# Performance work log

Hardware: AMD Instinct MI355X
Metric: run time of the kernel (lower is better)

## Reference

```python
import jax, jax.numpy as jnp
import numpy as np

NA, NH, E, EL, D = 100000, 20000, 1000000, 200000, 128


def _sage(x_src, x_dst, src, dst, W_l, b_l, W_r, num_dst):
    # PyG SAGEConv: out = lin_l(mean_j x_src[j]) + lin_r(x_dst); lin_l has bias, lin_r does not.
    msg = x_src[src]                                   # [E, D] gather
    agg = jax.ops.segment_sum(msg, dst, num_segments=num_dst)   # [num_dst, D]
    deg = jax.ops.segment_sum(jnp.ones((src.shape[0],), x_src.dtype), dst, num_segments=num_dst)
    agg = agg / jnp.maximum(deg, 1.0)[:, None]         # mean aggregation; isolated nodes -> 0
    return agg @ W_l + b_l + x_dst @ W_r


def setup_inputs() -> dict:
    key = jax.random.key(0)
    ks = jax.random.split(key, 24)
    s = 1.0 / np.sqrt(D)
    inp = {
        "x_author": jax.random.normal(ks[0], (NA, D), jnp.float32),
        "x_hotel": jax.random.normal(ks[1], (NH, D), jnp.float32),
        "ei_ah_src": jax.random.randint(ks[2], (E,), 0, NA, jnp.int32),
        "ei_ah_dst": jax.random.randint(ks[3], (E,), 0, NH, jnp.int32),
        "ei_ha_src": jax.random.randint(ks[4], (E,), 0, NH, jnp.int32),
        "ei_ha_dst": jax.random.randint(ks[5], (E,), 0, NA, jnp.int32),
        "eli_row": jax.random.randint(ks[6], (EL,), 0, NA, jnp.int32),
        "eli_col": jax.random.randint(ks[7], (EL,), 0, NH, jnp.int32),
    }
    # per-layer, per-edge-type SAGE weights
    names = ["W1_ah_l", "W1_ah_r", "W1_ha_l", "W1_ha_r", "W2_ah_l", "W2_ah_r", "W2_ha_l", "W2_ha_r"]
    for i, n in enumerate(names):
        inp[n] = jax.random.normal(ks[8 + i], (D, D), jnp.float32) * s
    inp["b1_ah_l"] = jnp.zeros((D,), jnp.float32)
    inp["b1_ha_l"] = jnp.zeros((D,), jnp.float32)
    inp["b2_ah_l"] = jnp.zeros((D,), jnp.float32)
    inp["b2_ha_l"] = jnp.zeros((D,), jnp.float32)
    # decoder MLP
    inp["W_lin1"] = jax.random.normal(ks[16], (2 * D, D), jnp.float32) * (1.0 / np.sqrt(2 * D))
    inp["b_lin1"] = jnp.zeros((D,), jnp.float32)
    inp["W_lin2"] = jax.random.normal(ks[17], (D, 1), jnp.float32) * s
    inp["b_lin2"] = jnp.zeros((1,), jnp.float32)
    return inp


def reference(x_author, x_hotel, ei_ah_src, ei_ah_dst, ei_ha_src, ei_ha_dst,
              eli_row, eli_col,
              W1_ah_l, b1_ah_l, W1_ah_r, W1_ha_l, b1_ha_l, W1_ha_r,
              W2_ah_l, b2_ah_l, W2_ah_r, W2_ha_l, b2_ha_l, W2_ha_r,
              W_lin1, b_lin1, W_lin2, b_lin2):
    # layer 1 (HeteroConv: each node type receives from exactly one edge type) + relu
    h_hotel = jax.nn.relu(_sage(x_author, x_hotel, ei_ah_src, ei_ah_dst, W1_ah_l, b1_ah_l, W1_ah_r, NH))
    h_author = jax.nn.relu(_sage(x_hotel, x_author, ei_ha_src, ei_ha_dst, W1_ha_l, b1_ha_l, W1_ha_r, NA))
    # layer 2 (no relu on last layer)
    z_hotel = _sage(h_author, h_hotel, ei_ah_src, ei_ah_dst, W2_ah_l, b2_ah_l, W2_ah_r, NH)
    z_author = _sage(h_hotel, h_author, ei_ha_src, ei_ha_dst, W2_ha_l, b2_ha_l, W2_ha_r, NA)
    # edge decoder: gather-concat -> 2-layer MLP
    z1 = jnp.concatenate([z_author[eli_row], z_hotel[eli_col]], axis=-1)  # [EL, 2D]
    z2 = jax.nn.relu(z1 @ W_lin1 + b_lin1)                                # [EL, D]
    pred = (z2 @ W_lin2 + b_lin2).reshape(-1)                             # [EL]
    return (pred, z1, z2)
```

## Files before the change

### kernel.cpp

```cpp
#include <hip/hip_runtime.h>

#define NA_ 100000
#define NH_ 20000
#define E_  1000000
#define EL_ 200000
#define D_  128

#define NBH_ 20
#define NBA_ 98
#define NBT_ 118

#define FBH_ 313
#define FBA_ 1563

typedef __attribute__((ext_vector_type(8))) short short8;
typedef __attribute__((ext_vector_type(4))) float f32x4;

__device__ __forceinline__ ushort f2bf(float f) {
  union { float f; uint u; } v; v.f = f;
  uint u = v.u;
  return (ushort)((u + 0x7FFFu + ((u >> 16) & 1u)) >> 16);
}
__device__ __forceinline__ uint pack2bf(float a, float b) {
  return (uint)f2bf(a) | ((uint)f2bf(b) << 16);
}


__global__ __launch_bounds__(256) void cvt_count_k(const float* __restrict__ xa, ushort* __restrict__ da,
                                                   const float* __restrict__ xh, ushort* __restrict__ dh,
                                                   const int* __restrict__ d1, int* __restrict__ c1,
                                                   const int* __restrict__ d2, int* __restrict__ c2) {
  int i = blockIdx.x * 256 + threadIdx.x;
  if (i < E_) atomicAdd(&c1[d1[i]], 1);
  else if (i < 2 * E_) atomicAdd(&c2[d2[i - E_]], 1);
  const int na4 = NA_ * 32;
  if (i < na4) {
    float4 v = *(const float4*)(xa + (size_t)i * 4);
    ((uint2*)da)[i] = make_uint2(pack2bf(v.x, v.y), pack2bf(v.z, v.w));
  } else {
    int k = i - na4;
    if (k < NH_ * 32) {
      float4 v = *(const float4*)(xh + (size_t)k * 4);
      ((uint2*)dh)[k] = make_uint2(pack2bf(v.x, v.y), pack2bf(v.z, v.w));
    }
  }
}


__global__ __launch_bounds__(256) void csr_partial_k(const int* __restrict__ cnt_h,
                                                     const int* __restrict__ cnt_a,
                                                     int* __restrict__ partials) {
  int b = blockIdx.x;
  bool isH = b < NBH_;
  const int* c = isH ? cnt_h : cnt_a;
  int n = isH ? NH_ : NA_;
  int chunk = isH ? b : b - NBH_;
  int t = threadIdx.x;
  int i0 = chunk * 1024 + t * 4;
  int s = 0;
  if (i0 + 3 < n) {
    int4 v = *(const int4*)(c + i0);
    s = v.x + v.y + v.z + v.w;
  } else {
    for (int k = 0; k < 4; k++) if (i0 + k < n) s += c[i0 + k];
  }
#pragma unroll
  for (int d = 1; d < 64; d <<= 1) s += __shfl_xor(s, d);
  __shared__ int ws[4];
  int lane = t & 63, wv = t >> 6;
  if (lane == 0) ws[wv] = s;
  __syncthreads();
  if (t == 0) partials[b] = ws[0] + ws[1] + ws[2] + ws[3];
}

__global__ __launch_bounds__(128) void csr_scanp_k(int* __restrict__ partials,
                                                   int* __restrict__ off_h,
                                                   int* __restrict__ off_a) {
  __shared__ int s[128];
  int t = threadIdx.x;
  int orig = (t < NBT_) ? partials[t] : 0;
  int seg = (t < NBH_) ? 0 : 1;
  s[t] = orig;
  __syncthreads();
  for (int d = 1; d < 128; d <<= 1) {
    int v = 0;
    if (t >= d) {
      int o = t - d;
      if (((o < NBH_) ? 0 : 1) == seg) v = s[o];
    }
    __syncthreads();
    s[t] += v;
    __syncthreads();
  }
  if (t < NBT_) partials[t] = s[t] - orig;
  if (t == 0) { off_h[NH_] = E_; off_a[NA_] = E_; }
}

__global__ __launch_bounds__(256) void csr_scatter_k(int* __restrict__ cnt_h, int* __restrict__ off_h,
                                                     int* __restrict__ cnt_a, int* __restrict__ off_a,
                                                     const int* __restrict__ partials) {
  int b = blockIdx.x;
  bool isH = b < NBH_;
  int* c = isH ? cnt_h : cnt_a;
  int* off = isH ? off_h : off_a;
  int n = isH ? NH_ : NA_;
  int chunk = isH ? b : b - NBH_;
  int t = threadIdx.x, lane = t & 63, wv = t >> 6;
  int base = partials[b];
  int i0 = chunk * 1024 + t * 4;
  int v0 = 0, v1 = 0, v2 = 0, v3 = 0;
  if (i0 + 3 < n) {
    int4 v = *(const int4*)(c + i0);
    v0 = v.x; v1 = v.y; v2 = v.z; v3 = v.w;
  } else {
    if (i0 < n) v0 = c[i0];
    if (i0 + 1 < n) v1 = c[i0 + 1];
    if (i0 + 2 < n) v2 = c[i0 + 2];
    if (i0 + 3 < n) v3 = c[i0 + 3];
  }
  int tsum = v0 + v1 + v2 + v3;
  int x = tsum;
#pragma unroll
  for (int d = 1; d < 64; d <<= 1) { int y = __shfl_up(x, d); if (lane >= d) x += y; }
  __shared__ int ws[4], wb[4];
  if (lane == 63) ws[wv] = x;
  __syncthreads();
  if (t == 0) { int r = 0; for (int i = 0; i < 4; i++) { wb[i] = r; r += ws[i]; } }
  __syncthreads();
  int run = base + wb[wv] + (x - tsum);
  int o0 = run, o1 = o0 + v0, o2 = o1 + v1, o3 = o2 + v2;
  if (i0 + 3 < n) {
    *(int4*)(off + i0) = make_int4(o0, o1, o2, o3);
    *(int4*)(c + i0) = make_int4(o0, o1, o2, o3);
  } else {
    if (i0 < n) { off[i0] = o0; c[i0] = o0; }
    if (i0 + 1 < n) { off[i0 + 1] = o1; c[i0 + 1] = o1; }
    if (i0 + 2 < n) { off[i0 + 2] = o2; c[i0 + 2] = o2; }
    if (i0 + 3 < n) { off[i0 + 3] = o3; c[i0 + 3] = o3; }
  }
}

__global__ void fill_edges_k(const int* __restrict__ s1, const int* __restrict__ d1,
                             int* __restrict__ cur1, int* __restrict__ out1,
                             const int* __restrict__ s2, const int* __restrict__ d2,
                             int* __restrict__ cur2, int* __restrict__ out2) {
  int i = blockIdx.x * 256 + threadIdx.x;
  if (i < E_) {
    int p = atomicAdd(&cur1[d1[i]], 1);
    out1[p] = s1[i];
  } else if (i < 2 * E_) {
    int ii = i - E_;
    int p = atomicAdd(&cur2[d2[ii]], 1);
    out2[p] = s2[ii];
  }
}


__global__ void pack_all_k(const float* a0, const float* a1, ushort* ad,
                           const float* b0, const float* b1, ushort* bd,
                           const float* c0, const float* c1, ushort* cd,
                           const float* d0, const float* d1, ushort* dd,
                           const float* e0, const float* e1, ushort* ed) {
  const float *s0, *s1; ushort* dst;
  switch (blockIdx.y) {
    case 0: s0 = a0; s1 = a1; dst = ad; break;
    case 1: s0 = b0; s1 = b1; dst = bd; break;
    case 2: s0 = c0; s1 = c1; dst = cd; break;
    case 3: s0 = d0; s1 = d1; dst = dd; break;
    default: s0 = e0; s1 = e1; dst = ed; break;
  }
  int idx = blockIdx.x * 256 + threadIdx.x;
  int j = idx & 7, lane = (idx >> 3) & 63, nt = (idx >> 9) & 7, kc = idx >> 12;
  int k = kc * 32 + (lane >> 4) * 8 + j;
  int n = nt * 16 + (lane & 15);
  float v = (k < 128) ? s0[k * 128 + n] : s1[(k - 128) * 128 + n];
  dst[idx] = f2bf(v);
}


template <bool RELU, bool OUTBF>
__global__ __launch_bounds__(256) void sage_fused_k(
    const int* __restrict__ off0, const int* __restrict__ src0,
    const ushort* __restrict__ G0, const ushort* __restrict__ X0,
    const ushort* __restrict__ W0, const float* __restrict__ B0,
    ushort* __restrict__ oB0, float* __restrict__ oF0, int n0, int nb0,
    const int* __restrict__ off1, const int* __restrict__ src1,
    const ushort* __restrict__ G1, const ushort* __restrict__ X1,
    const ushort* __restrict__ W1, const float* __restrict__ B1,
    ushort* __restrict__ oB1, float* __restrict__ oF1, int n1) {
  const int b = blockIdx.x;
  const bool p0 = b < nb0;
  const int* off = p0 ? off0 : off1;
  const int* srcs = p0 ? src0 : src1;
  const ushort* G = p0 ? G0 : G1;
  const ushort* X = p0 ? X0 : X1;
  const ushort* Wp = p0 ? W0 : W1;
  const float* bias = p0 ? B0 : B1;
  ushort* outB = p0 ? oB0 : oB1;
  float* outF = p0 ? oF0 : oF1;
  const int rows = p0 ? n0 : n1;
  const int rb = (p0 ? b : b - nb0) * 64;

  __shared__ ushort At[64 * 136];

  const int t = threadIdx.x, w = t >> 6, lane = t & 63;
  const int grp = lane >> 4, sub = lane & 15;
  const ushort* gbase = G + sub * 8;

  for (int rr = 0; rr < 16; rr++) {
    int row = rb + w * 16 + rr;
    float a[8] = {0.f, 0.f, 0.f, 0.f, 0.f, 0.f, 0.f, 0.f};
    int deg = 0;
    if (row < rows) {
      int beg = off[row], end = off[row + 1];
      deg = end - beg;
      int j = beg + grp;
      for (; j + 4 < end; j += 8) {
        int sA = srcs[j];
        int sB = srcs[j + 4];
        uint4 vA = *(const uint4*)(gbase + (size_t)sA * 128);
        uint4 vB = *(const uint4*)(gbase + (size_t)sB * 128);
        a[0] += __uint_as_float(vA.x << 16); a[1] += __uint_as_float(vA.x & 0xFFFF0000u);
        a[2] += __uint_as_float(vA.y << 16); a[3] += __uint_as_float(vA.y & 0xFFFF0000u);
        a[4] += __uint_as_float(vA.z << 16); a[5] += __uint_as_float(vA.z & 0xFFFF0000u);
        a[6] += __uint_as_float(vA.w << 16); a[7] += __uint_as_float(vA.w & 0xFFFF0000u);
        a[0] += __uint_as_float(vB.x << 16); a[1] += __uint_as_float(vB.x & 0xFFFF0000u);
        a[2] += __uint_as_float(vB.y << 16); a[3] += __uint_as_float(vB.y & 0xFFFF0000u);
        a[4] += __uint_as_float(vB.z << 16); a[5] += __uint_as_float(vB.z & 0xFFFF0000u);
        a[6] += __uint_as_float(vB.w << 16); a[7] += __uint_as_float(vB.w & 0xFFFF0000u);
      }
      if (j < end) {
        int sA = srcs[j];
        uint4 vA = *(const uint4*)(gbase + (size_t)sA * 128);
        a[0] += __uint_as_float(vA.x << 16); a[1] += __uint_as_float(vA.x & 0xFFFF0000u);
        a[2] += __uint_as_float(vA.y << 16); a[3] += __uint_as_float(vA.y & 0xFFFF0000u);
        a[4] += __uint_as_float(vA.z << 16); a[5] += __uint_as_float(vA.z & 0xFFFF0000u);
        a[6] += __uint_as_float(vA.w << 16); a[7] += __uint_as_float(vA.w & 0xFFFF0000u);
      }
#pragma unroll
      for (int k = 0; k < 8; k++) {
        a[k] += __shfl_xor(a[k], 16);
        a[k] += __shfl_xor(a[k], 32);
      }
    }
    if (grp == 0) {
      float sc = 1.0f / (float)(deg > 0 ? deg : 1);
      uint4 o;
      o.x = pack2bf(a[0] * sc, a[1] * sc);
      o.y = pack2bf(a[2] * sc, a[3] * sc);
      o.z = pack2bf(a[4] * sc, a[5] * sc);
      o.w = pack2bf(a[6] * sc, a[7] * sc);
      *(uint4*)(At + (w * 16 + rr) * 136 + sub * 8) = o;
    }
  }
  __syncthreads();

  const int quad = lane >> 4, m = lane & 15;
  int rA = rb + w * 16 + m; if (rA >= rows) rA = rows - 1;
  f32x4 acc[8];
#pragma unroll
  for (int nt = 0; nt < 8; nt++) acc[nt] = (f32x4){0.f, 0.f, 0.f, 0.f};
#pragma unroll
  for (int kc = 0; kc < 8; kc++) {
    short8 a;
    if (kc < 4) a = *(const short8*)(At + (w * 16 + m) * 136 + kc * 32 + quad * 8);
    else        a = *(const short8*)(X + (size_t)rA * 128 + (kc - 4) * 32 + quad * 8);
    const ushort* wp = Wp + (size_t)(kc * 8) * 512 + lane * 8;
#pragma unroll
    for (int nt = 0; nt < 8; nt++) {
      short8 bfr = *(const short8*)(wp + nt * 512);
      acc[nt] = __builtin_amdgcn_mfma_f32_16x16x32_bf16(a, bfr, acc[nt], 0, 0, 0);
    }
  }
#pragma unroll
  for (int nt = 0; nt < 8; nt++) {
    float bv = bias[nt * 16 + m];
#pragma unroll
    for (int r = 0; r < 4; r++) {
      int row = rb + w * 16 + quad * 4 + r;
      if (row < rows) {
        float v = acc[nt][r] + bv;
        if (RELU) v = fmaxf(v, 0.f);
        if (OUTBF) outB[(size_t)row * 128 + nt * 16 + m] = f2bf(v);
        else       outF[(size_t)row * 128 + nt * 16 + m] = v;
      }
    }
  }
}


__global__ __launch_bounds__(256) void decoder_mfma_k(const float* __restrict__ Za,
                                                      const float* __restrict__ Zh,
                                                      const int* __restrict__ rowi,
                                                      const int* __restrict__ coli,
                                                      const ushort* __restrict__ Wp,
                                                      const float* __restrict__ b1,
                                                      const float* __restrict__ W2,
                                                      const float* __restrict__ b2,
                                                      float* __restrict__ pred,
                                                      float* __restrict__ z1o,
                                                      float* __restrict__ z2o) {
  __shared__ ushort z1bf[64 * 264];
  __shared__ int ra[64], rc[64];
  const int t = threadIdx.x, w = t >> 6, lane = t & 63, quad = lane >> 4, m = lane & 15;
  const int rb = blockIdx.x * 64;
  if (t < 64) ra[t] = rowi[rb + t];
  else if (t < 128) rc[t - 64] = coli[rb + t - 64];
  __syncthreads();
#pragma unroll 4
  for (int rr = 0; rr < 16; rr++) {
    int row = w * 16 + rr;
    int a = ra[row], c = rc[row];
    float2 va = *(const float2*)(Za + (size_t)a * 128 + lane * 2);
    float2 vc = *(const float2*)(Zh + (size_t)c * 128 + lane * 2);
    float* zr = z1o + (size_t)(rb + row) * 256;
    __builtin_nontemporal_store(*(const double*)&va, (double*)(zr + lane * 2));
    __builtin_nontemporal_store(*(const double*)&vc, (double*)(zr + 128 + lane * 2));
    uint* lbase = (uint*)(z1bf + row * 264);
    lbase[lane] = pack2bf(va.x, va.y);
    lbase[64 + lane] = pack2bf(vc.x, vc.y);
  }
  __syncthreads();
  f32x4 acc[8];
#pragma unroll
  for (int nt = 0; nt < 8; nt++) acc[nt] = (f32x4){0.f, 0.f, 0.f, 0.f};
#pragma unroll
  for (int kc = 0; kc < 8; kc++) {
    short8 a = *(const short8*)(z1bf + (w * 16 + m) * 264 + kc * 32 + quad * 8);
    const ushort* wp = Wp + (size_t)(kc * 8) * 512 + lane * 8;
#pragma unroll
    for (int nt = 0; nt < 8; nt++) {
      short8 b = *(const short8*)(wp + nt * 512);
      acc[nt] = __builtin_amdgcn_mfma_f32_16x16x32_bf16(a, b, acc[nt], 0, 0, 0);
    }
  }
  float part[4] = {0.f, 0.f, 0.f, 0.f};
#pragma unroll
  for (int nt = 0; nt < 8; nt++) {
    float bv = b1[nt * 16 + m];
    float wv = W2[nt * 16 + m];
#pragma unroll
    for (int r = 0; r < 4; r++) {
      float v = fmaxf(acc[nt][r] + bv, 0.f);
      __builtin_nontemporal_store(v, z2o + (size_t)(rb + w * 16 + quad * 4 + r) * 128 + nt * 16 + m);
      part[r] += v * wv;
    }
  }
  const float bias2 = b2[0];
#pragma unroll
  for (int r = 0; r < 4; r++) {
    float s = part[r];
    s += __shfl_xor(s, 1); s += __shfl_xor(s, 2);
    s += __shfl_xor(s, 4); s += __shfl_xor(s, 8);
    if (m == 0) pred[rb + w * 16 + quad * 4 + r] = s + bias2;
  }
}


static inline char* carve(char*& p, size_t bytes) {
  char* r = p;
  p += (bytes + 255) & ~(size_t)255;
  return r;
}

extern "C" void kernel_launch(void* const* d_in, const int* in_sizes, int n_in,
                              void* d_out, int out_size, void* d_ws, size_t ws_size,
                              hipStream_t stream) {
  const float* x_author = (const float*)d_in[0];
  const float* x_hotel  = (const float*)d_in[1];
  const int* ei_ah_src  = (const int*)d_in[2];
  const int* ei_ah_dst  = (const int*)d_in[3];
  const int* ei_ha_src  = (const int*)d_in[4];
  const int* ei_ha_dst  = (const int*)d_in[5];
  const int* eli_row    = (const int*)d_in[6];
  const int* eli_col    = (const int*)d_in[7];
  const float* W1_ah_l  = (const float*)d_in[8];
  const float* W1_ah_r  = (const float*)d_in[9];
  const float* W1_ha_l  = (const float*)d_in[10];
  const float* W1_ha_r  = (const float*)d_in[11];
  const float* W2_ah_l  = (const float*)d_in[12];
  const float* W2_ah_r  = (const float*)d_in[13];
  const float* W2_ha_l  = (const float*)d_in[14];
  const float* W2_ha_r  = (const float*)d_in[15];
  const float* b1_ah_l  = (const float*)d_in[16];
  const float* b1_ha_l  = (const float*)d_in[17];
  const float* b2_ah_l  = (const float*)d_in[18];
  const float* b2_ha_l  = (const float*)d_in[19];
  const float* W_lin1   = (const float*)d_in[20];
  const float* b_lin1   = (const float*)d_in[21];
  const float* W_lin2   = (const float*)d_in[22];
  const float* b_lin2   = (const float*)d_in[23];

  char* p = (char*)d_ws;
  ushort* xa_bf = (ushort*)carve(p, (size_t)NA_ * D_ * 2);
  ushort* xh_bf = (ushort*)carve(p, (size_t)NH_ * D_ * 2);
  ushort* H_hbf = (ushort*)carve(p, (size_t)NH_ * D_ * 2);
  ushort* H_abf = (ushort*)carve(p, (size_t)NA_ * D_ * 2);
  float*  Z_h   = (float*)carve(p, (size_t)NH_ * D_ * 4);
  float*  Z_a   = (float*)carve(p, (size_t)NA_ * D_ * 4);
  ushort* Wp1ah = (ushort*)carve(p, 32768 * 2);
  ushort* Wp1ha = (ushort*)carve(p, 32768 * 2);
  ushort* Wp2ah = (ushort*)carve(p, 32768 * 2);
  ushort* Wp2ha = (ushort*)carve(p, 32768 * 2);
  ushort* WpD   = (ushort*)carve(p, 32768 * 2);
  int* off_h = (int*)carve(p, (size_t)(NH_ + 1) * 4);
  int* off_a = (int*)carve(p, (size_t)(NA_ + 1) * 4);
  int* cur_h = (int*)carve(p, (size_t)(NH_ + NA_) * 4);
  int* cur_a = cur_h + NH_;
  int* s_ah  = (int*)carve(p, (size_t)E_ * 4);
  int* s_ha  = (int*)carve(p, (size_t)E_ * 4);
  int* partials = (int*)carve(p, 256 * 4);

  float* pred = (float*)d_out;
  float* z1o  = pred + EL_;
  float* z2o  = z1o + (size_t)EL_ * 256;

  hipMemsetAsync(cur_h, 0, (size_t)(NH_ + NA_) * 4, stream);
  cvt_count_k<<<(NA_ * 32 + NH_ * 32 + 255) / 256, 256, 0, stream>>>(
      x_author, xa_bf, x_hotel, xh_bf, ei_ah_dst, cur_h, ei_ha_dst, cur_a);

  csr_partial_k<<<NBT_, 256, 0, stream>>>(cur_h, cur_a, partials);
  csr_scanp_k<<<1, 128, 0, stream>>>(partials, off_h, off_a);
  csr_scatter_k<<<NBT_, 256, 0, stream>>>(cur_h, off_h, cur_a, off_a, partials);

  fill_edges_k<<<(2 * E_ + 255) / 256, 256, 0, stream>>>(ei_ah_src, ei_ah_dst, cur_h, s_ah,
                                                         ei_ha_src, ei_ha_dst, cur_a, s_ha);

  dim3 pg(128, 5);
  pack_all_k<<<pg, 256, 0, stream>>>(W1_ah_l, W1_ah_r, Wp1ah,
                                     W1_ha_l, W1_ha_r, Wp1ha,
                                     W2_ah_l, W2_ah_r, Wp2ah,
                                     W2_ha_l, W2_ha_r, Wp2ha,
                                     W_lin1, W_lin1 + 128 * 128, WpD);

  sage_fused_k<true, true><<<FBH_ + FBA_, 256, 0, stream>>>(
      off_h, s_ah, xa_bf, xh_bf, Wp1ah, b1_ah_l, H_hbf, nullptr, NH_, FBH_,
      off_a, s_ha, xh_bf, xa_bf, Wp1ha, b1_ha_l, H_abf, nullptr, NA_);

  sage_fused_k<false, false><<<FBH_ + FBA_, 256, 0, stream>>>(
      off_h, s_ah, H_abf, H_hbf, Wp2ah, b2_ah_l, nullptr, Z_h, NH_, FBH_,
      off_a, s_ha, H_hbf, H_abf, Wp2ha, b2_ha_l, nullptr, Z_a, NA_);

  decoder_mfma_k<<<EL_ / 64, 256, 0, stream>>>(Z_a, Z_h, eli_row, eli_col,
                                               WpD, b_lin1, W_lin2, b_lin2,
                                               pred, z1o, z2o);
}
```

Baseline: 890.1 us.

## Assign one row per 16-lane group in SAGE aggregation; widen decoder gathers

The fused SAGE aggregate+GEMM kernel now gives each 16-lane group its own destination row, so the four groups of a wave process four rows at once. This removes the cross-group shuffle reduction, and the inner loop is unrolled over four neighbours. The X fragments for the root-term MFMA are prefetched into registers before aggregation so their latency overlaps the gathers. The decoder gather now uses 16-byte loads and stores per lane, with half the wave reading each source. Per-row work is now uneven across groups when degrees differ, and register pressure goes up.

```diff
diff --git a/kernel.cpp b/kernel.cpp
--- a/kernel.cpp
+++ b/kernel.cpp
@@ -23,6 +23,12 @@
 }
 __device__ __forceinline__ uint pack2bf(float a, float b) {
   return (uint)f2bf(a) | ((uint)f2bf(b) << 16);
+}
+__device__ __forceinline__ void acc8(float* a, const uint4& v) {
+  a[0] += __uint_as_float(v.x << 16); a[1] += __uint_as_float(v.x & 0xFFFF0000u);
+  a[2] += __uint_as_float(v.y << 16); a[3] += __uint_as_float(v.y & 0xFFFF0000u);
+  a[4] += __uint_as_float(v.z << 16); a[5] += __uint_as_float(v.z & 0xFFFF0000u);
+  a[6] += __uint_as_float(v.w << 16); a[7] += __uint_as_float(v.w & 0xFFFF0000u);
 }
 
 
@@ -205,58 +211,46 @@
 
   const int t = threadIdx.x, w = t >> 6, lane = t & 63;
   const int grp = lane >> 4, sub = lane & 15;
+  const int quad = lane >> 4, m = lane & 15;
   const ushort* gbase = G + sub * 8;
 
-  for (int rr = 0; rr < 16; rr++) {
+  int rA = rb + w * 16 + m; if (rA >= rows) rA = rows - 1;
+  short8 xfrag[4];
+#pragma unroll
+  for (int kk = 0; kk < 4; kk++)
+    xfrag[kk] = *(const short8*)(X + (size_t)rA * 128 + kk * 32 + quad * 8);
+
+  for (int rr = grp; rr < 16; rr += 4) {
     int row = rb + w * 16 + rr;
     float a[8] = {0.f, 0.f, 0.f, 0.f, 0.f, 0.f, 0.f, 0.f};
     int deg = 0;
     if (row < rows) {
       int beg = off[row], end = off[row + 1];
       deg = end - beg;
-      int j = beg + grp;
-      for (; j + 4 < end; j += 8) {
-        int sA = srcs[j];
-        int sB = srcs[j + 4];
-        uint4 vA = *(const uint4*)(gbase + (size_t)sA * 128);
-        uint4 vB = *(const uint4*)(gbase + (size_t)sB * 128);
-        a[0] += __uint_as_float(vA.x << 16); a[1] += __uint_as_float(vA.x & 0xFFFF0000u);
-        a[2] += __uint_as_float(vA.y << 16); a[3] += __uint_as_float(vA.y & 0xFFFF0000u);
-        a[4] += __uint_as_float(vA.z << 16); a[5] += __uint_as_float(vA.z & 0xFFFF0000u);
-        a[6] += __uint_as_float(vA.w << 16); a[7] += __uint_as_float(vA.w & 0xFFFF0000u);
-        a[0] += __uint_as_float(vB.x << 16); a[1] += __uint_as_float(vB.x & 0xFFFF0000u);
-        a[2] += __uint_as_float(vB.y << 16); a[3] += __uint_as_float(vB.y & 0xFFFF0000u);
-        a[4] += __uint_as_float(vB.z << 16); a[5] += __uint_as_float(vB.z & 0xFFFF0000u);
-        a[6] += __uint_as_float(vB.w << 16); a[7] += __uint_as_float(vB.w & 0xFFFF0000u);
+      int j = beg;
+      for (; j + 3 < end; j += 4) {
+        int s0 = srcs[j], s1 = srcs[j + 1], s2 = srcs[j + 2], s3 = srcs[j + 3];
+        uint4 v0 = *(const uint4*)(gbase + (size_t)s0 * 128);
+        uint4 v1 = *(const uint4*)(gbase + (size_t)s1 * 128);
+        uint4 v2 = *(const uint4*)(gbase + (size_t)s2 * 128);
+        uint4 v3 = *(const uint4*)(gbase + (size_t)s3 * 128);
+        acc8(a, v0); acc8(a, v1); acc8(a, v2); acc8(a, v3);
       }
-      if (j < end) {
-        int sA = srcs[j];
-        uint4 vA = *(const uint4*)(gbase + (size_t)sA * 128);
-        a[0] += __uint_as_float(vA.x << 16); a[1] += __uint_as_float(vA.x & 0xFFFF0000u);
-        a[2] += __uint_as_float(vA.y << 16); a[3] += __uint_as_float(vA.y & 0xFFFF0000u);
-        a[4] += __uint_as_float(vA.z << 16); a[5] += __uint_as_float(vA.z & 0xFFFF0000u);
-        a[6] += __uint_as_float(vA.w << 16); a[7] += __uint_as_float(vA.w & 0xFFFF0000u);
+      for (; j < end; j++) {
+        uint4 v = *(const uint4*)(gbase + (size_t)srcs[j] * 128);
+        acc8(a, v);
       }
-#pragma unroll
-      for (int k = 0; k < 8; k++) {
-        a[k] += __shfl_xor(a[k], 16);
-        a[k] += __shfl_xor(a[k], 32);
-      }
-    }
-    if (grp == 0) {
-      float sc = 1.0f / (float)(deg > 0 ? deg : 1);
-      uint4 o;
-      o.x = pack2bf(a[0] * sc, a[1] * sc);
-      o.y = pack2bf(a[2] * sc, a[3] * sc);
-      o.z = pack2bf(a[4] * sc, a[5] * sc);
-      o.w = pack2bf(a[6] * sc, a[7] * sc);
-      *(uint4*)(At + (w * 16 + rr) * 136 + sub * 8) = o;
-    }
-  }
-  __syncthreads();
-
-  const int quad = lane >> 4, m = lane & 15;
-  int rA = rb + w * 16 + m; if (rA >= rows) rA = rows - 1;
+    }
+    float sc = 1.0f / (float)(deg > 0 ? deg : 1);
+    uint4 o;
+    o.x = pack2bf(a[0] * sc, a[1] * sc);
+    o.y = pack2bf(a[2] * sc, a[3] * sc);
+    o.z = pack2bf(a[4] * sc, a[5] * sc);
+    o.w = pack2bf(a[6] * sc, a[7] * sc);
+    *(uint4*)(At + (w * 16 + rr) * 136 + sub * 8) = o;
+  }
+  __syncthreads();
+
   f32x4 acc[8];
 #pragma unroll
   for (int nt = 0; nt < 8; nt++) acc[nt] = (f32x4){0.f, 0.f, 0.f, 0.f};
@@ -264,7 +258,7 @@
   for (int kc = 0; kc < 8; kc++) {
     short8 a;
     if (kc < 4) a = *(const short8*)(At + (w * 16 + m) * 136 + kc * 32 + quad * 8);
-    else        a = *(const short8*)(X + (size_t)rA * 128 + (kc - 4) * 32 + quad * 8);
+    else        a = xfrag[kc - 4];
     const ushort* wp = Wp + (size_t)(kc * 8) * 512 + lane * 8;
 #pragma unroll
     for (int nt = 0; nt < 8; nt++) {
@@ -307,18 +301,19 @@
   if (t < 64) ra[t] = rowi[rb + t];
   else if (t < 128) rc[t - 64] = coli[rb + t - 64];
   __syncthreads();
+  const int half = lane >> 5, hl = lane & 31;
 #pragma unroll 4
   for (int rr = 0; rr < 16; rr++) {
     int row = w * 16 + rr;
-    int a = ra[row], c = rc[row];
-    float2 va = *(const float2*)(Za + (size_t)a * 128 + lane * 2);
-    float2 vc = *(const float2*)(Zh + (size_t)c * 128 + lane * 2);
-    float* zr = z1o + (size_t)(rb + row) * 256;
-    __builtin_nontemporal_store(*(const double*)&va, (double*)(zr + lane * 2));
-    __builtin_nontemporal_store(*(const double*)&vc, (double*)(zr + 128 + lane * 2));
-    uint* lbase = (uint*)(z1bf + row * 264);
-    lbase[lane] = pack2bf(va.x, va.y);
-    lbase[64 + lane] = pack2bf(vc.x, vc.y);
+    const float* srcp = half ? (Zh + (size_t)rc[row] * 128 + hl * 4)
+                             : (Za + (size_t)ra[row] * 128 + hl * 4);
+    f32x4 v = *(const f32x4*)srcp;
+    float* zr = z1o + (size_t)(rb + row) * 256 + half * 128 + hl * 4;
+    __builtin_nontemporal_store(v, (f32x4*)zr);
+    uint2 pk;
+    pk.x = pack2bf(v.x, v.y);
+    pk.y = pack2bf(v.z, v.w);
+    *(uint2*)(z1bf + row * 264 + half * 128 + hl * 4) = pk;
   }
   __syncthreads();
   f32x4 acc[8];
```

Result: no change. 898.0 us (+0.9%).
